# Optimization experiments

Measured on AMD Instinct MI355X. Metric: run time of the kernel, lower is better.

The kernel has to match this reference:

```python
import jax, jax.numpy as jnp
import numpy as np

N = 100000       # num nodes
E = 3200000      # num edges
F_IN = 32        # num_node_features
F_EDGE = 16      # num_edge_features
H = 27           # hidden_dim
OUT = 1          # output_dim


def setup_inputs() -> dict:
    key = jax.random.key(0)
    ks = jax.random.split(key, 12)
    inp = {
        "x": jax.random.normal(ks[0], (N, F_IN), dtype=jnp.float32),
        "edge_index": jax.random.randint(ks[1], (2, E), 0, N, dtype=jnp.int64),
        "edge_attr": jax.random.normal(ks[2], (E, F_EDGE), dtype=jnp.float32),
        # GCNConv layer params (PyG uses weight [in, out] applied as x @ W)
        "W1": jax.random.normal(ks[3], (F_IN, H), dtype=jnp.float32) * (1.0 / np.sqrt(F_IN)),
        "b1": jnp.zeros((H,), dtype=jnp.float32),
        "W2": jax.random.normal(ks[4], (H, H), dtype=jnp.float32) * (1.0 / np.sqrt(H)),
        "b2": jnp.zeros((H,), dtype=jnp.float32),
        # edge MLP
        "ew1": jax.random.normal(ks[5], (F_EDGE, H), dtype=jnp.float32) * (1.0 / np.sqrt(F_EDGE)),
        "eb1": jnp.zeros((H,), dtype=jnp.float32),
        "ew2": jax.random.normal(ks[6], (H, H), dtype=jnp.float32) * (1.0 / np.sqrt(H)),
        "eb2": jnp.zeros((H,), dtype=jnp.float32),
        # final edge head: in = 2*H + H = 3*H
        "fcw": jax.random.normal(ks[7], (3 * H, OUT), dtype=jnp.float32) * (1.0 / np.sqrt(3 * H)),
        "fcb": jnp.zeros((OUT,), dtype=jnp.float32),
    }
    return inp


def gcn_conv(x, edge_index, W, b):
    # PyG GCNConv with add_self_loops=True, symmetric normalization.
    row, col = edge_index[0], edge_index[1]
    loops = jnp.arange(N, dtype=edge_index.dtype)
    row_sl = jnp.concatenate([row, loops])  # sources
    col_sl = jnp.concatenate([col, loops])  # targets
    # degree computed on target nodes (edge weights = 1)
    deg = jax.ops.segment_sum(jnp.ones_like(col_sl, dtype=x.dtype), col_sl, num_segments=N)
    dinv = jnp.where(deg > 0, jax.lax.rsqrt(deg), 0.0)
    norm = dinv[row_sl] * dinv[col_sl]  # [E+N]
    h = x @ W  # [N, H]
    msg = h[row_sl] * norm[:, None]  # gather + scale
    out = jax.ops.segment_sum(msg, col_sl, num_segments=N)  # scatter-add
    return out + b


def reference(x, edge_index, edge_attr, W1, b1, W2, b2, ew1, eb1, ew2, eb2, fcw, fcb):
    h = jax.nn.relu(gcn_conv(x, edge_index, W1, b1))
    # dropout is identity in eval mode (training=False)
    h = gcn_conv(h, edge_index, W2, b2)
    ef = jax.nn.relu(edge_attr @ ew1 + eb1) @ ew2 + eb2  # [E, H]
    row, col = edge_index[0], edge_index[1]
    emb = jnp.concatenate([h[row], h[col], ef], axis=1)  # [E, 3H]
    pred = (emb @ fcw + fcb).squeeze()  # [E]
    return pred
```

## Files before the change

kernel.cpp:

```cpp
#include <hip/hip_runtime.h>

#define N_NODES 100000
#define N_EDGES 3200000
#define F_IN 32
#define F_EDGE 16
#define H 27
#define PAD 32
#define NB_NODES 391
#define NBUCK 391
#define BCAP 9216
#define CHUNK 12500

__global__ __launch_bounds__(256) void k_initcur(int* __restrict__ cursor) {
    int i = blockIdx.x * 256 + threadIdx.x;
    if (i < NBUCK) cursor[i] = i * BCAP;
}

__global__ __launch_bounds__(1024) void k_bin(const int* __restrict__ ei,
                                              int* __restrict__ cursor,
                                              int* __restrict__ binned) {
    __shared__ int stage[CHUNK];
    __shared__ int hist[NBUCK];
    __shared__ int bstart[NBUCK];
    __shared__ int gbase[NBUCK];
    __shared__ int scanbuf[512];
    int tid = threadIdx.x;
    long long cs = (long long)blockIdx.x * CHUNK;

    for (int i = tid; i < NBUCK; i += 1024) hist[i] = 0;
    __syncthreads();

    int pk[13], bk[13], rk[13];
#pragma unroll
    for (int i = 0; i < 13; i++) {
        int j = tid + i * 1024;
        bk[i] = -1;
        if (j < CHUNK) {
            int e = (int)(cs + j);
            int r = ei[e];
            int c = ei[N_EDGES + e];
            int b = c >> 8;
            pk[i] = (r << 8) | (c & 255);
            bk[i] = b;
            rk[i] = atomicAdd(&hist[b], 1);
        }
    }
    __syncthreads();

    if (tid < 512) scanbuf[tid] = (tid < NBUCK) ? hist[tid] : 0;
    __syncthreads();
    for (int off = 1; off < 512; off <<= 1) {
        int v = 0;
        if (tid < 512 && tid >= off) v = scanbuf[tid - off];
        __syncthreads();
        if (tid < 512) scanbuf[tid] += v;
        __syncthreads();
    }
    if (tid < NBUCK) {
        bstart[tid] = scanbuf[tid] - hist[tid];
        gbase[tid] = (hist[tid] > 0) ? atomicAdd(&cursor[tid], hist[tid]) : 0;
    }
    __syncthreads();

#pragma unroll
    for (int i = 0; i < 13; i++) {
        if (bk[i] >= 0) stage[bstart[bk[i]] + rk[i]] = pk[i];
    }
    __syncthreads();

    for (int j = tid; j < CHUNK; j += 1024) {
        int lo = 0, hi = NBUCK - 1;
        while (lo < hi) {
            int mid = (lo + hi + 1) >> 1;
            if (bstart[mid] <= j) lo = mid; else hi = mid - 1;
        }
        binned[gbase[lo] + (j - bstart[lo])] = stage[j];
    }
}

__global__ __launch_bounds__(512) void k_bscan(const int* __restrict__ cursor,
                                               int* __restrict__ bbase,
                                               int* __restrict__ ptr) {
    __shared__ int sb[512];
    int tid = threadIdx.x;
    int cnt = (tid < NBUCK) ? (cursor[tid] - tid * BCAP) : 0;
    sb[tid] = cnt;
    __syncthreads();
    for (int off = 1; off < 512; off <<= 1) {
        int t = (tid >= off) ? sb[tid - off] : 0;
        __syncthreads();
        sb[tid] += t;
        __syncthreads();
    }
    if (tid < NBUCK) bbase[tid] = sb[tid] - cnt;
    if (tid == NBUCK - 1) ptr[N_NODES] = sb[tid];
}

__global__ __launch_bounds__(256) void k_bin2(const int* __restrict__ cursor,
                                              const int* __restrict__ binned,
                                              const int* __restrict__ bbase,
                                              int* __restrict__ ptr,
                                              int* __restrict__ csr,
                                              float* __restrict__ dinv) {
    __shared__ int hist[256];
    __shared__ int offs[256];
    __shared__ int stage[BCAP];
    int b = blockIdx.x, tid = threadIdx.x;
    hist[tid] = 0;
    __syncthreads();
    int base = b * BCAP;
    int cnt = cursor[b] - base;
    int gb = bbase[b];

    int recs[36], rks[36];
#pragma unroll
    for (int i = 0; i < 36; i++) {
        int j = tid + i * 256;
        recs[i] = -1;
        if (j < cnt) {
            int rec = binned[base + j];
            recs[i] = rec;
            rks[i] = atomicAdd(&hist[rec & 255], 1);
        }
    }
    __syncthreads();

    int v = hist[tid];
    offs[tid] = v;
    __syncthreads();
    for (int off = 1; off < 256; off <<= 1) {
        int t = (tid >= off) ? offs[tid - off] : 0;
        __syncthreads();
        offs[tid] += t;
        __syncthreads();
    }
    int excl = offs[tid] - v;
    int n = b * 256 + tid;
    if (n < N_NODES) {
        ptr[n] = gb + excl;
        dinv[n] = rsqrtf((float)(v + 1));
    }
    __syncthreads();
    offs[tid] = excl;
    __syncthreads();

#pragma unroll
    for (int i = 0; i < 36; i++) {
        if (recs[i] >= 0) stage[offs[recs[i] & 255] + rks[i]] = recs[i] >> 8;
    }
    __syncthreads();
    for (int j = tid; j < cnt; j += 256) csr[gb + j] = stage[j];
}

__global__ __launch_bounds__(256) void k_l1pre(const float* __restrict__ x,
                                               const float* __restrict__ W1,
                                               const float* __restrict__ dinv,
                                               float* __restrict__ bufA) {
    __shared__ float w[F_IN * H];
    for (int i = threadIdx.x; i < F_IN * H; i += 256) w[i] = W1[i];
    __syncthreads();
    int n = blockIdx.x * 256 + threadIdx.x;
    if (n >= N_NODES) return;

    float xv[F_IN];
    const float4* xp = (const float4*)(x + (long long)n * F_IN);
#pragma unroll
    for (int j = 0; j < F_IN / 4; j++) {
        float4 v = xp[j];
        xv[4 * j] = v.x; xv[4 * j + 1] = v.y; xv[4 * j + 2] = v.z; xv[4 * j + 3] = v.w;
    }
    float di = dinv[n];
    long long base = (long long)n * PAD;
#pragma unroll
    for (int j = 0; j < H; j++) {
        float acc = 0.f;
#pragma unroll
        for (int k = 0; k < F_IN; k++) acc += xv[k] * w[k * H + j];
        bufA[base + j] = acc * di;
    }
}

__global__ __launch_bounds__(256) void k_gather_post(const int* __restrict__ ptr,
                                                     const int* __restrict__ csr,
                                                     const float* __restrict__ bufA,
                                                     const float* __restrict__ W2,
                                                     const float* __restrict__ b1,
                                                     const float* __restrict__ fcw,
                                                     const float* __restrict__ dinv,
                                                     float2* __restrict__ s01) {
    __shared__ float w[H * H];
    __shared__ float bs[H], f0[H], f1[H];
    for (int i = threadIdx.x; i < H * H; i += 256) w[i] = W2[i];
    if (threadIdx.x < H) {
        bs[threadIdx.x] = b1[threadIdx.x];
        f0[threadIdx.x] = fcw[threadIdx.x];
        f1[threadIdx.x] = fcw[H + threadIdx.x];
    }
    __syncthreads();

    int g = blockIdx.x * 256 + threadIdx.x;
    int n = g >> 5;
    int lane = g & 31;
    if (n >= N_NODES) return;
    int p0 = ptr[n], p1 = ptr[n + 1];

    float acc = (lane < H) ? bufA[(long long)n * PAD + lane] : 0.f;
    int i = p0;
    while (i < p1) {
        int m = p1 - i; if (m > 32) m = 32;
        int idx = (lane < m) ? csr[i + lane] : 0;
#pragma unroll 4
        for (int j = 0; j < m; j++) {
            int r = __shfl(idx, j, 32);
            acc += bufA[(long long)r * PAD + lane];
        }
        i += m;
    }

    float di = dinv[n];
    float o1 = 0.f;
    if (lane < H) {
        float t = bs[lane] + di * acc;
        o1 = t > 0.f ? t : 0.f;
    }
    float gj = 0.f;
#pragma unroll
    for (int k = 0; k < H; k++) {
        float ok = __shfl(o1, k, 32);
        if (lane < H) gj += ok * w[k * H + lane];
    }
    float t0 = 0.f, t1 = 0.f;
    if (lane < H) {
        float gd = gj * di;
        t0 = gd * f0[lane];
        t1 = gd * f1[lane];
    }
#pragma unroll
    for (int off = 16; off > 0; off >>= 1) {
        t0 += __shfl_xor(t0, off, 32);
        t1 += __shfl_xor(t1, off, 32);
    }
    if (lane == 0) s01[n] = make_float2(t0, t1);
}

__global__ void k_prep(const float* __restrict__ ew2,
                       const float* __restrict__ eb2,
                       const float* __restrict__ b2,
                       const float* __restrict__ fcw,
                       const float* __restrict__ fcb,
                       float* __restrict__ vbuf) {
    int k = threadIdx.x;
    if (k < H) {
        float acc = 0.f;
#pragma unroll
        for (int j = 0; j < H; j++) acc += ew2[k * H + j] * fcw[2 * H + j];
        vbuf[k] = acc;
    } else if (k == H) {
        float acc = fcb[0];
#pragma unroll
        for (int j = 0; j < H; j++) acc += eb2[j] * fcw[2 * H + j];
        vbuf[H] = acc;
    } else if (k == H + 1) {
        float acc = 0.f;
#pragma unroll
        for (int j = 0; j < H; j++) acc += b2[j] * fcw[j];
        vbuf[H + 1] = acc;
    } else if (k == H + 2) {
        float acc = 0.f;
#pragma unroll
        for (int j = 0; j < H; j++) acc += b2[j] * fcw[H + j];
        vbuf[H + 2] = acc;
    }
}

__global__ __launch_bounds__(256) void k_pull2(const int* __restrict__ ptr,
                                               const int* __restrict__ csr,
                                               const float2* __restrict__ s01,
                                               const float* __restrict__ dinv,
                                               const float* __restrict__ vbuf,
                                               float* __restrict__ pr,
                                               float* __restrict__ pc) {
    int g = blockIdx.x * 256 + threadIdx.x;
    int n = g >> 5;
    int lane = g & 31;
    if (n >= N_NODES) return;
    int p0 = ptr[n], p1 = ptr[n + 1];

    float a0 = 0.f, a1 = 0.f;
    for (int i = p0 + lane; i < p1; i += 32) {
        float2 s = s01[csr[i]];
        a0 += s.x;
        a1 += s.y;
    }
#pragma unroll
    for (int off = 16; off > 0; off >>= 1) {
        a0 += __shfl_down(a0, off, 32);
        a1 += __shfl_down(a1, off, 32);
    }
    if (lane == 0) {
        float2 ss = s01[n];
        float di = dinv[n];
        pr[n] = vbuf[H + 1] + di * (a0 + ss.x);
        pc[n] = vbuf[H + 2] + di * (a1 + ss.y);
    }
}

__global__ __launch_bounds__(256) void k_edge_final(const int* __restrict__ ei,
                                                    const float* __restrict__ ea,
                                                    const float* __restrict__ ew1,
                                                    const float* __restrict__ eb1,
                                                    const float* __restrict__ vbuf,
                                                    const float* __restrict__ pr,
                                                    const float* __restrict__ pc,
                                                    float* __restrict__ out) {
    __shared__ float w1t[H * F_EDGE];
    __shared__ float2 bv[H];
    __shared__ float c0s;
    for (int i = threadIdx.x; i < H * F_EDGE; i += 256) {
        int k = i >> 4, m = i & 15;
        w1t[i] = ew1[m * H + k];
    }
    if (threadIdx.x < H) bv[threadIdx.x] = make_float2(eb1[threadIdx.x], vbuf[threadIdx.x]);
    if (threadIdx.x == 0) c0s = vbuf[H];
    __syncthreads();

    long long t = (long long)blockIdx.x * 256 + threadIdx.x;
    long long e0 = t * 2;
    if (e0 >= N_EDGES) return;

    int2 rr = *(const int2*)(ei + e0);
    int2 cc = *(const int2*)(ei + N_EDGES + e0);
    float g0 = pr[rr.x];
    float g1 = pr[rr.y];
    float h0 = pc[cc.x];
    float h1 = pc[cc.y];

    float a[2][F_EDGE];
#pragma unroll
    for (int i = 0; i < 2; i++) {
        const float4* p = (const float4*)(ea + (e0 + i) * F_EDGE);
#pragma unroll
        for (int j = 0; j < F_EDGE / 4; j++) {
            float4 v = p[j];
            a[i][4 * j] = v.x; a[i][4 * j + 1] = v.y; a[i][4 * j + 2] = v.z; a[i][4 * j + 3] = v.w;
        }
    }

    float c0 = c0s;
    float acc0 = c0, acc1 = c0;
    const float4* w1v = (const float4*)w1t;
#pragma unroll
    for (int k = 0; k < H; k++) {
        float4 wa = w1v[k * 4 + 0];
        float4 wb = w1v[k * 4 + 1];
        float4 wc = w1v[k * 4 + 2];
        float4 wd = w1v[k * 4 + 3];
        float2 bvk = bv[k];
        float s0 = bvk.x;
        s0 += a[0][0] * wa.x + a[0][1] * wa.y + a[0][2] * wa.z + a[0][3] * wa.w;
        s0 += a[0][4] * wb.x + a[0][5] * wb.y + a[0][6] * wb.z + a[0][7] * wb.w;
        s0 += a[0][8] * wc.x + a[0][9] * wc.y + a[0][10] * wc.z + a[0][11] * wc.w;
        s0 += a[0][12] * wd.x + a[0][13] * wd.y + a[0][14] * wd.z + a[0][15] * wd.w;
        float s1 = bvk.x;
        s1 += a[1][0] * wa.x + a[1][1] * wa.y + a[1][2] * wa.z + a[1][3] * wa.w;
        s1 += a[1][4] * wb.x + a[1][5] * wb.y + a[1][6] * wb.z + a[1][7] * wb.w;
        s1 += a[1][8] * wc.x + a[1][9] * wc.y + a[1][10] * wc.z + a[1][11] * wc.w;
        s1 += a[1][12] * wd.x + a[1][13] * wd.y + a[1][14] * wd.z + a[1][15] * wd.w;
        acc0 += (s0 > 0.f ? s0 : 0.f) * bvk.y;
        acc1 += (s1 > 0.f ? s1 : 0.f) * bvk.y;
    }

    acc0 += g0 + h0;
    acc1 += g1 + h1;
    *(float2*)(out + e0) = make_float2(acc0, acc1);
}

extern "C" void kernel_launch(void* const* d_in, const int* in_sizes, int n_in,
                              void* d_out, int out_size, void* d_ws, size_t ws_size,
                              hipStream_t stream) {
    const float* x   = (const float*)d_in[0];
    const int*   ei  = (const int*)d_in[1];
    const float* ea  = (const float*)d_in[2];
    const float* W1  = (const float*)d_in[3];
    const float* b1  = (const float*)d_in[4];
    const float* W2  = (const float*)d_in[5];
    const float* b2  = (const float*)d_in[6];
    const float* ew1 = (const float*)d_in[7];
    const float* eb1 = (const float*)d_in[8];
    const float* ew2 = (const float*)d_in[9];
    const float* eb2 = (const float*)d_in[10];
    const float* fcw = (const float*)d_in[11];
    const float* fcb = (const float*)d_in[12];
    float* out = (float*)d_out;

    int* cursor  = (int*)d_ws;
    int* bbase   = cursor + 1024;
    int* binned  = bbase + 512;
    int* ptr     = binned + (size_t)NBUCK * BCAP;
    int* csr     = ptr + N_NODES + 1024;
    float* dinv  = (float*)(csr + N_EDGES);
    float* bufA  = dinv + N_NODES;
    float2* s01  = (float2*)(bufA + (size_t)N_NODES * PAD);
    float* pr    = (float*)(s01 + N_NODES);
    float* pc    = pr + N_NODES;
    float* vbuf  = pc + N_NODES;

    const int nb_ng = (N_NODES * 32 + 255) / 256;
    const int nb_e2 = N_EDGES / 2 / 256;

    k_initcur<<<2, 256, 0, stream>>>(cursor);
    k_bin<<<256, 1024, 0, stream>>>(ei, cursor, binned);
    k_bscan<<<1, 512, 0, stream>>>(cursor, bbase, ptr);
    k_bin2<<<NBUCK, 256, 0, stream>>>(cursor, binned, bbase, ptr, csr, dinv);

    k_prep<<<1, 64, 0, stream>>>(ew2, eb2, b2, fcw, fcb, vbuf);

    k_l1pre<<<NB_NODES, 256, 0, stream>>>(x, W1, dinv, bufA);
    k_gather_post<<<nb_ng, 256, 0, stream>>>(ptr, csr, bufA, W2, b1, fcw, dinv, s01);

    k_pull2<<<nb_ng, 256, 0, stream>>>(ptr, csr, s01, dinv, vbuf, pr, pc);

    k_edge_final<<<nb_e2, 256, 0, stream>>>(ei, ea, ew1, eb1, vbuf, pr, pc, out);
}
```

Before: 539.0 us.

## Replace CSR build with bucket-binned aggregation using shared-memory atomics

```diff
diff --git a/kernel.cpp b/kernel.cpp
--- a/kernel.cpp
+++ b/kernel.cpp
@@ -11,14 +11,47 @@
 #define BCAP 9216
 #define CHUNK 12500
 
-__global__ __launch_bounds__(256) void k_initcur(int* __restrict__ cursor) {
-    int i = blockIdx.x * 256 + threadIdx.x;
-    if (i < NBUCK) cursor[i] = i * BCAP;
+__global__ __launch_bounds__(1024) void k_prep(const float* __restrict__ ew2,
+                                               const float* __restrict__ eb2,
+                                               const float* __restrict__ b2,
+                                               const float* __restrict__ fcw,
+                                               const float* __restrict__ fcb,
+                                               float* __restrict__ vbuf,
+                                               int* __restrict__ cursor,
+                                               int* __restrict__ deg) {
+    int g = blockIdx.x * 1024 + threadIdx.x;
+    if (g < N_NODES) deg[g] = 0;
+    if (blockIdx.x == 0) {
+        int k = threadIdx.x;
+        if (k < NBUCK) cursor[k] = k * BCAP;
+        if (k < H) {
+            float acc = 0.f;
+#pragma unroll
+            for (int j = 0; j < H; j++) acc += ew2[k * H + j] * fcw[2 * H + j];
+            vbuf[k] = acc;
+        } else if (k == H) {
+            float acc = fcb[0];
+#pragma unroll
+            for (int j = 0; j < H; j++) acc += eb2[j] * fcw[2 * H + j];
+            vbuf[H] = acc;
+        } else if (k == H + 1) {
+            float acc = 0.f;
+#pragma unroll
+            for (int j = 0; j < H; j++) acc += b2[j] * fcw[j];
+            vbuf[H + 1] = acc;
+        } else if (k == H + 2) {
+            float acc = 0.f;
+#pragma unroll
+            for (int j = 0; j < H; j++) acc += b2[j] * fcw[H + j];
+            vbuf[H + 2] = acc;
+        }
+    }
 }
 
 __global__ __launch_bounds__(1024) void k_bin(const int* __restrict__ ei,
                                               int* __restrict__ cursor,
-                                              int* __restrict__ binned) {
+                                              int* __restrict__ binned,
+                                              int* __restrict__ deg) {
     __shared__ int stage[CHUNK];
     __shared__ int hist[NBUCK];
     __shared__ int bstart[NBUCK];
@@ -43,6 +76,7 @@
             pk[i] = (r << 8) | (c & 255);
             bk[i] = b;
             rk[i] = atomicAdd(&hist[b], 1);
+            atomicAdd(&deg[c], 1);
         }
     }
     __syncthreads();
@@ -68,93 +102,22 @@
     }
     __syncthreads();
 
-    for (int j = tid; j < CHUNK; j += 1024) {
-        int lo = 0, hi = NBUCK - 1;
-        while (lo < hi) {
-            int mid = (lo + hi + 1) >> 1;
-            if (bstart[mid] <= j) lo = mid; else hi = mid - 1;
-        }
-        binned[gbase[lo] + (j - bstart[lo])] = stage[j];
-    }
-}
-
-__global__ __launch_bounds__(512) void k_bscan(const int* __restrict__ cursor,
-                                               int* __restrict__ bbase,
-                                               int* __restrict__ ptr) {
-    __shared__ int sb[512];
-    int tid = threadIdx.x;
-    int cnt = (tid < NBUCK) ? (cursor[tid] - tid * BCAP) : 0;
-    sb[tid] = cnt;
-    __syncthreads();
-    for (int off = 1; off < 512; off <<= 1) {
-        int t = (tid >= off) ? sb[tid - off] : 0;
-        __syncthreads();
-        sb[tid] += t;
-        __syncthreads();
-    }
-    if (tid < NBUCK) bbase[tid] = sb[tid] - cnt;
-    if (tid == NBUCK - 1) ptr[N_NODES] = sb[tid];
-}
-
-__global__ __launch_bounds__(256) void k_bin2(const int* __restrict__ cursor,
-                                              const int* __restrict__ binned,
-                                              const int* __restrict__ bbase,
-                                              int* __restrict__ ptr,
-                                              int* __restrict__ csr,
-                                              float* __restrict__ dinv) {
-    __shared__ int hist[256];
-    __shared__ int offs[256];
-    __shared__ int stage[BCAP];
-    int b = blockIdx.x, tid = threadIdx.x;
-    hist[tid] = 0;
-    __syncthreads();
-    int base = b * BCAP;
-    int cnt = cursor[b] - base;
-    int gb = bbase[b];
-
-    int recs[36], rks[36];
-#pragma unroll
-    for (int i = 0; i < 36; i++) {
-        int j = tid + i * 256;
-        recs[i] = -1;
-        if (j < cnt) {
-            int rec = binned[base + j];
-            recs[i] = rec;
-            rks[i] = atomicAdd(&hist[rec & 255], 1);
-        }
-    }
-    __syncthreads();
-
-    int v = hist[tid];
-    offs[tid] = v;
-    __syncthreads();
-    for (int off = 1; off < 256; off <<= 1) {
-        int t = (tid >= off) ? offs[tid - off] : 0;
-        __syncthreads();
-        offs[tid] += t;
-        __syncthreads();
-    }
-    int excl = offs[tid] - v;
-    int n = b * 256 + tid;
-    if (n < N_NODES) {
-        ptr[n] = gb + excl;
-        dinv[n] = rsqrtf((float)(v + 1));
-    }
-    __syncthreads();
-    offs[tid] = excl;
-    __syncthreads();
-
-#pragma unroll
-    for (int i = 0; i < 36; i++) {
-        if (recs[i] >= 0) stage[offs[recs[i] & 255] + rks[i]] = recs[i] >> 8;
-    }
-    __syncthreads();
-    for (int j = tid; j < cnt; j += 256) csr[gb + j] = stage[j];
+    int lane = tid & 31;
+    int grp = tid >> 5;
+    for (int b = grp; b < NBUCK; b += 32) {
+        int cnt = hist[b];
+        if (cnt == 0) continue;
+        int s = bstart[b];
+        int g = gbase[b];
+        for (int l = lane; l < cnt; l += 32)
+            binned[g + l] = stage[s + l];
+    }
 }
 
 __global__ __launch_bounds__(256) void k_l1pre(const float* __restrict__ x,
                                                const float* __restrict__ W1,
-                                               const float* __restrict__ dinv,
+                                               const int* __restrict__ deg,
+                                               float* __restrict__ dinv,
                                                float* __restrict__ bufA) {
     __shared__ float w[F_IN * H];
     for (int i = threadIdx.x; i < F_IN * H; i += 256) w[i] = W1[i];
@@ -169,139 +132,131 @@
         float4 v = xp[j];
         xv[4 * j] = v.x; xv[4 * j + 1] = v.y; xv[4 * j + 2] = v.z; xv[4 * j + 3] = v.w;
     }
-    float di = dinv[n];
-    long long base = (long long)n * PAD;
+    float di = rsqrtf((float)(deg[n] + 1));
+    dinv[n] = di;
+    float ov[PAD];
 #pragma unroll
     for (int j = 0; j < H; j++) {
         float acc = 0.f;
 #pragma unroll
         for (int k = 0; k < F_IN; k++) acc += xv[k] * w[k * H + j];
-        bufA[base + j] = acc * di;
-    }
-}
-
-__global__ __launch_bounds__(256) void k_gather_post(const int* __restrict__ ptr,
-                                                     const int* __restrict__ csr,
-                                                     const float* __restrict__ bufA,
-                                                     const float* __restrict__ W2,
-                                                     const float* __restrict__ b1,
-                                                     const float* __restrict__ fcw,
-                                                     const float* __restrict__ dinv,
-                                                     float2* __restrict__ s01) {
+        ov[j] = acc * di;
+    }
+#pragma unroll
+    for (int j = H; j < PAD; j++) ov[j] = 0.f;
+    float4* op = (float4*)(bufA + (long long)n * PAD);
+#pragma unroll
+    for (int j = 0; j < PAD / 4; j++)
+        op[j] = make_float4(ov[4 * j], ov[4 * j + 1], ov[4 * j + 2], ov[4 * j + 3]);
+}
+
+__global__ __launch_bounds__(512) void k_agg1(const int* __restrict__ cursor,
+                                              const int* __restrict__ binned,
+                                              const float* __restrict__ bufA,
+                                              const float* __restrict__ W2,
+                                              const float* __restrict__ b1,
+                                              const float* __restrict__ fcw,
+                                              const float* __restrict__ dinv,
+                                              float2* __restrict__ s01) {
+    __shared__ float acc[256 * 32];
     __shared__ float w[H * H];
     __shared__ float bs[H], f0[H], f1[H];
-    for (int i = threadIdx.x; i < H * H; i += 256) w[i] = W2[i];
-    if (threadIdx.x < H) {
-        bs[threadIdx.x] = b1[threadIdx.x];
-        f0[threadIdx.x] = fcw[threadIdx.x];
-        f1[threadIdx.x] = fcw[H + threadIdx.x];
-    }
-    __syncthreads();
-
-    int g = blockIdx.x * 256 + threadIdx.x;
-    int n = g >> 5;
-    int lane = g & 31;
-    if (n >= N_NODES) return;
-    int p0 = ptr[n], p1 = ptr[n + 1];
-
-    float acc = (lane < H) ? bufA[(long long)n * PAD + lane] : 0.f;
-    int i = p0;
-    while (i < p1) {
-        int m = p1 - i; if (m > 32) m = 32;
-        int idx = (lane < m) ? csr[i + lane] : 0;
-#pragma unroll 4
-        for (int j = 0; j < m; j++) {
-            int r = __shfl(idx, j, 32);
-            acc += bufA[(long long)r * PAD + lane];
-        }
-        i += m;
-    }
-
-    float di = dinv[n];
-    float o1 = 0.f;
-    if (lane < H) {
-        float t = bs[lane] + di * acc;
-        o1 = t > 0.f ? t : 0.f;
-    }
-    float gj = 0.f;
-#pragma unroll
-    for (int k = 0; k < H; k++) {
-        float ok = __shfl(o1, k, 32);
-        if (lane < H) gj += ok * w[k * H + lane];
-    }
-    float t0 = 0.f, t1 = 0.f;
-    if (lane < H) {
-        float gd = gj * di;
-        t0 = gd * f0[lane];
-        t1 = gd * f1[lane];
-    }
-#pragma unroll
-    for (int off = 16; off > 0; off >>= 1) {
-        t0 += __shfl_xor(t0, off, 32);
-        t1 += __shfl_xor(t1, off, 32);
-    }
-    if (lane == 0) s01[n] = make_float2(t0, t1);
-}
-
-__global__ void k_prep(const float* __restrict__ ew2,
-                       const float* __restrict__ eb2,
-                       const float* __restrict__ b2,
-                       const float* __restrict__ fcw,
-                       const float* __restrict__ fcb,
-                       float* __restrict__ vbuf) {
-    int k = threadIdx.x;
-    if (k < H) {
-        float acc = 0.f;
-#pragma unroll
-        for (int j = 0; j < H; j++) acc += ew2[k * H + j] * fcw[2 * H + j];
-        vbuf[k] = acc;
-    } else if (k == H) {
-        float acc = fcb[0];
-#pragma unroll
-        for (int j = 0; j < H; j++) acc += eb2[j] * fcw[2 * H + j];
-        vbuf[H] = acc;
-    } else if (k == H + 1) {
-        float acc = 0.f;
-#pragma unroll
-        for (int j = 0; j < H; j++) acc += b2[j] * fcw[j];
-        vbuf[H + 1] = acc;
-    } else if (k == H + 2) {
-        float acc = 0.f;
-#pragma unroll
-        for (int j = 0; j < H; j++) acc += b2[j] * fcw[H + j];
-        vbuf[H + 2] = acc;
-    }
-}
-
-__global__ __launch_bounds__(256) void k_pull2(const int* __restrict__ ptr,
-                                               const int* __restrict__ csr,
-                                               const float2* __restrict__ s01,
-                                               const float* __restrict__ dinv,
-                                               const float* __restrict__ vbuf,
-                                               float* __restrict__ pr,
-                                               float* __restrict__ pc) {
-    int g = blockIdx.x * 256 + threadIdx.x;
-    int n = g >> 5;
-    int lane = g & 31;
-    if (n >= N_NODES) return;
-    int p0 = ptr[n], p1 = ptr[n + 1];
-
-    float a0 = 0.f, a1 = 0.f;
-    for (int i = p0 + lane; i < p1; i += 32) {
-        float2 s = s01[csr[i]];
-        a0 += s.x;
-        a1 += s.y;
-    }
-#pragma unroll
-    for (int off = 16; off > 0; off >>= 1) {
-        a0 += __shfl_down(a0, off, 32);
-        a1 += __shfl_down(a1, off, 32);
-    }
-    if (lane == 0) {
+    int tid = threadIdx.x;
+    int b = blockIdx.x;
+    for (int i = tid; i < 256 * 32; i += 512) acc[i] = 0.f;
+    for (int i = tid; i < H * H; i += 512) w[i] = W2[i];
+    if (tid < H) {
+        bs[tid] = b1[tid];
+        f0[tid] = fcw[tid];
+        f1[tid] = fcw[H + tid];
+    }
+    __syncthreads();
+
+    int base = b * BCAP;
+    int cnt = cursor[b] - base;
+    int q = tid & 7;
+    int rsub = tid >> 3;
+
+    for (int it = 0; it < cnt; it += 64) {
+        int rid = it + rsub;
+        if (rid < cnt) {
+            int rec = binned[base + rid];
+            int row = rec >> 8;
+            int slot = rec & 255;
+            float4 v = ((const float4*)(bufA + (long long)row * PAD))[q];
+            int bi = slot * 32;
+            atomicAdd(&acc[bi + ((4 * q + 0 + slot) & 31)], v.x);
+            atomicAdd(&acc[bi + ((4 * q + 1 + slot) & 31)], v.y);
+            atomicAdd(&acc[bi + ((4 * q + 2 + slot) & 31)], v.z);
+            atomicAdd(&acc[bi + ((4 * q + 3 + slot) & 31)], v.w);
+        }
+    }
+    __syncthreads();
+
+    int lane = tid & 31;
+    int grp = tid >> 5;
+    for (int s = grp; s < 256; s += 16) {
+        int n = b * 256 + s;
+        if (n >= N_NODES) continue;
+        float a = acc[s * 32 + ((lane + s) & 31)];
+        a += bufA[(long long)n * PAD + lane];
+        float di = dinv[n];
+        float o1 = 0.f;
+        if (lane < H) {
+            float t = bs[lane] + di * a;
+            o1 = t > 0.f ? t : 0.f;
+        }
+        float gj = 0.f;
+#pragma unroll
+        for (int k = 0; k < H; k++) {
+            float ok = __shfl(o1, k, 32);
+            if (lane < H) gj += ok * w[k * H + lane];
+        }
+        float t0 = 0.f, t1 = 0.f;
+        if (lane < H) {
+            float gd = gj * di;
+            t0 = gd * f0[lane];
+            t1 = gd * f1[lane];
+        }
+#pragma unroll
+        for (int off = 16; off > 0; off >>= 1) {
+            t0 += __shfl_xor(t0, off, 32);
+            t1 += __shfl_xor(t1, off, 32);
+        }
+        if (lane == 0) s01[n] = make_float2(t0, t1);
+    }
+}
+
+__global__ __launch_bounds__(256) void k_agg2(const int* __restrict__ cursor,
+                                              const int* __restrict__ binned,
+                                              const float2* __restrict__ s01,
+                                              const float* __restrict__ dinv,
+                                              const float* __restrict__ vbuf,
+                                              float* __restrict__ pr,
+                                              float* __restrict__ pc) {
+    __shared__ float ax[256], ay[256];
+    int tid = threadIdx.x;
+    int b = blockIdx.x;
+    ax[tid] = 0.f;
+    ay[tid] = 0.f;
+    __syncthreads();
+
+    int base = b * BCAP;
+    int cnt = cursor[b] - base;
+    for (int it = tid; it < cnt; it += 256) {
+        int rec = binned[base + it];
+        float2 s = s01[rec >> 8];
+        atomicAdd(&ax[rec & 255], s.x);
+        atomicAdd(&ay[rec & 255], s.y);
+    }
+    __syncthreads();
+
+    int n = b * 256 + tid;
+    if (n < N_NODES) {
         float2 ss = s01[n];
         float di = dinv[n];
-        pr[n] = vbuf[H + 1] + di * (a0 + ss.x);
-        pc[n] = vbuf[H + 2] + di * (a1 + ss.y);
+        pr[n] = vbuf[H + 1] + di * (ax[tid] + ss.x);
+        pc[n] = vbuf[H + 2] + di * (ay[tid] + ss.y);
     }
 }
 
@@ -397,28 +352,24 @@
     int* bbase   = cursor + 1024;
     int* binned  = bbase + 512;
     int* ptr     = binned + (size_t)NBUCK * BCAP;
-    int* csr     = ptr + N_NODES + 1024;
-    float* dinv  = (float*)(csr + N_EDGES);
+    int* deg     = ptr + N_NODES + 1024;
+    float* dinv  = (float*)(deg + N_EDGES);
     float* bufA  = dinv + N_NODES;
     float2* s01  = (float2*)(bufA + (size_t)N_NODES * PAD);
     float* pr    = (float*)(s01 + N_NODES);
     float* pc    = pr + N_NODES;
     float* vbuf  = pc + N_NODES;
 
-    const int nb_ng = (N_NODES * 32 + 255) / 256;
     const int nb_e2 = N_EDGES / 2 / 256;
 
-    k_initcur<<<2, 256, 0, stream>>>(cursor);
-    k_bin<<<256, 1024, 0, stream>>>(ei, cursor, binned);
-    k_bscan<<<1, 512, 0, stream>>>(cursor, bbase, ptr);
-    k_bin2<<<NBUCK, 256, 0, stream>>>(cursor, binned, bbase, ptr, csr, dinv);
-
-    k_prep<<<1, 64, 0, stream>>>(ew2, eb2, b2, fcw, fcb, vbuf);
-
-    k_l1pre<<<NB_NODES, 256, 0, stream>>>(x, W1, dinv, bufA);
-    k_gather_post<<<nb_ng, 256, 0, stream>>>(ptr, csr, bufA, W2, b1, fcw, dinv, s01);
-
-    k_pull2<<<nb_ng, 256, 0, stream>>>(ptr, csr, s01, dinv, vbuf, pr, pc);
+    k_prep<<<98, 1024, 0, stream>>>(ew2, eb2, b2, fcw, fcb, vbuf, cursor, deg);
+
+    k_bin<<<256, 1024, 0, stream>>>(ei, cursor, binned, deg);
+
+    k_l1pre<<<NB_NODES, 256, 0, stream>>>(x, W1, deg, dinv, bufA);
+
+    k_agg1<<<NBUCK, 512, 0, stream>>>(cursor, binned, bufA, W2, b1, fcw, dinv, s01);
+    k_agg2<<<NBUCK, 256, 0, stream>>>(cursor, binned, s01, dinv, vbuf, pr, pc);
 
     k_edge_final<<<nb_e2, 256, 0, stream>>>(ei, ea, ew1, eb1, vbuf, pr, pc, out);
 }
```

Result: slower. 1.241 ms (+130.3%).
